# Kernel tuning notes

Hardware: AMD Instinct MI355X
Metric: run time of the kernel (lower is better)

Reference implementation:

```python
import jax, jax.numpy as jnp
import numpy as np

M_RANGE = 3
K = 2 * M_RANGE + 1          # kernel size = 7
N_CLASS = K * K              # 49 motion classes
IM_CHANNEL = 3


def setup_inputs() -> dict:
    key = jax.random.key(0)
    k1, k2, k3, k4 = jax.random.split(key, 4)
    B, H, W = 16, 256, 256
    im_input = jax.random.normal(k1, (B, 2 * IM_CHANNEL, H, W), dtype=jnp.float32)
    im_output = jax.random.normal(k2, (B, IM_CHANNEL, H, W), dtype=jnp.float32)
    # motion in [-M_RANGE, M_RANGE-1) so that floor(m)+M_RANGE+1 <= K-1 (valid bin)
    gt_motion = jax.random.uniform(k3, (B, 2, H, W), dtype=jnp.float32) * (2 * M_RANGE - 1) - M_RANGE
    # grouped-conv weight (already in post-swapaxes [n_class, 1, K, K] layout)
    m_kernel = jax.random.uniform(k4, (N_CLASS, 1, K, K), dtype=jnp.float32)
    return {"im_input": im_input, "im_output": im_output,
            "gt_motion": gt_motion, "m_kernel": m_kernel}


def _axis_weights(m):
    # m: [B,H,W] -> bilinear binning weights over K bins: [B,H,W,K]
    f = jnp.floor(m)
    frac = m - f
    idx = f.astype(jnp.int32) + M_RANGE
    oh0 = jax.nn.one_hot(idx, K, dtype=m.dtype)
    oh1 = jax.nn.one_hot(idx + 1, K, dtype=m.dtype)
    return (1.0 - frac)[..., None] * oh0 + frac[..., None] * oh1


def motion2mask(motion):
    # faithful vectorization of the triple-loop: mask[c=iy*K+ix] = b[iy]*a[ix]
    ax = _axis_weights(motion[:, 0])   # x-motion -> columns of ger(b, a)
    ay = _axis_weights(motion[:, 1])   # y-motion -> rows
    mask = ay[..., :, None] * ax[..., None, :]       # [B,H,W,K,K] outer product
    B, H, W = motion.shape[0], motion.shape[2], motion.shape[3]
    return mask.reshape(B, H, W, N_CLASS).transpose(0, 3, 1, 2)  # [B,N_CLASS,H,W]


def _conv(x, w, groups):
    return jax.lax.conv_general_dilated(
        x, w, window_strides=(1, 1),
        padding=[(M_RANGE, M_RANGE), (M_RANGE, M_RANGE)],
        dimension_numbers=("NCHW", "OIHW", "NCHW"),
        feature_group_count=groups)


def reference(im_input, im_output, gt_motion, m_kernel):
    m_mask = motion2mask(gt_motion)                   # [B,N_CLASS,H,W]
    out_mask = _conv(m_mask, m_kernel, N_CLASS)       # grouped conv, same shape
    im = im_input[:, -IM_CHANNEL:]                    # [B,3,H,W]
    B, C, H, W = im.shape
    # construct_image: each channel expanded to N_CLASS copies then grouped-conv
    # == plain conv of each single channel with all N_CLASS kernels
    nearby = _conv(im.reshape(B * C, 1, H, W), m_kernel, 1)
    nearby = nearby.reshape(B, C, N_CLASS, H, W)
    pred = (nearby * out_mask[:, None]).sum(axis=2)   # [B,3,H,W]
    return pred, m_mask
```

## Files before the change

kernel.cpp:

```cpp
#include <hip/hip_runtime.h>
#include <hip/hip_fp16.h>

typedef _Float16 f16x8 __attribute__((ext_vector_type(8)));
typedef float    f32x4 __attribute__((ext_vector_type(4)));

#define TILE   16
#define HALO   22
#define KK     7
#define NCLASS 49
#define IMW    256
#define IMH    256
#define HW     65536
#define HH     484
#define NV     42
#define WROW   34

#define OFF_OMV    0
#define OFF_HALOF  10752
#define OFF_HALOB  11236
#define OFF_KV     11360
#define SH_TOTAL   13424
#define OFF_IML64  10752
#define OFF_IML32  11720

#define WS_B    0
#define WS_KV   3072
#define WS_KV4  (3072/4)

__device__ __forceinline__ unsigned h2u(__half2 h) { union { __half2 h; unsigned u; } c; c.h = h; return c.u; }
__device__ __forceinline__ __half2  u2h(unsigned u) { union { __half2 h; unsigned u; } c; c.u = u; return c.h; }

__global__ void gtnet_setup(const float* __restrict__ m_kernel, unsigned* __restrict__ ws)
{
    const int tid = threadIdx.x;
    for (int idx = tid; idx < 768; idx += 256) {
        int lane = idx & 63, kitnt = idx >> 6;
        int kit = kitnt >> 2, nt = kitnt & 3;
        int vb0 = (lane >> 4) * 4, tcol = lane & 15;
        int t = nt * 16 + tcol; int tc = (t > 48) ? 48 : t;
        uint4 o;
        unsigned* op = (unsigned*)&o;
        #pragma unroll
        for (int j = 0; j < 4; j++) {
            int v = kit * 16 + vb0 + j;
            float lo = (v <= 41) ? m_kernel[v * NCLASS + tc]        : 0.0f;
            float hi = (v <= 41) ? m_kernel[(v + KK) * NCLASS + tc] : 0.0f;
            op[j] = h2u(__halves2half2(__float2half_rn(lo), __float2half_rn(hi)));
        }
        ((uint4*)ws)[idx] = o;
    }
    for (int i = tid; i < 2064; i += 256) {
        unsigned val = 0u;
        if (i < NCLASS * NV) {
            int s = i / NV, n = i - s * NV;
            val = h2u(__halves2half2(__float2half_rn(m_kernel[n * NCLASS + s]),
                                     __float2half_rn(m_kernel[(n + KK) * NCLASS + s])));
        }
        ws[WS_KV + i] = val;
    }
}

__global__ __launch_bounds__(256, 3)
void gtnet_kernel(const float* __restrict__ im_input,
                  const float* __restrict__ gt_motion,
                  float* __restrict__ out_pred,
                  float* __restrict__ out_mask,
                  const unsigned* __restrict__ ws)
{
    __shared__ __align__(16) unsigned SH[SH_TOTAL];
    unsigned*      const omV    = SH + OFF_OMV;
    unsigned*      const haloF  = SH + OFF_HALOF;
    unsigned char* const haloB8 = (unsigned char*)(SH + OFF_HALOB);
    unsigned*      const KV     = SH + OFF_KV;
    float2*        const iml64  = (float2*)(SH + OFF_IML64);
    float*         const iml32  = (float*)(SH + OFF_IML32);

    const int tid  = threadIdx.x;
    const int lane = tid & 63, wv_id = tid >> 6;
    const int tx = tid & 15, ty = tid >> 4;
    const int x0 = blockIdx.x * TILE, y0 = blockIdx.y * TILE;
    const int b  = blockIdx.z;
    const int x = x0 + tx, y = y0 + ty;

    const float* mot_x = gt_motion + (size_t)b * 2 * HW;
    const float* mot_y = mot_x + HW;
    const float* imP   = im_input + ((size_t)b * 6 + 3) * HW;

    float2 imr01[2]; float imr2[2];
    #pragma unroll
    for (int k = 0; k < 2; k++) {
        int i = tid + k * 256;
        float2 v01 = make_float2(0.0f, 0.0f); float v2 = 0.0f;
        if (i < HH) {
            int hy = i / HALO, hx = i - hy * HALO;
            int gy = y0 - 3 + hy, gx = x0 - 3 + hx;
            if (gy >= 0 && gy < IMH && gx >= 0 && gx < IMW) {
                int off = gy * IMW + gx;
                v01.x = imP[off];
                v01.y = imP[off + HW];
                v2    = imP[off + 2 * HW];
            }
        }
        imr01[k] = v01; imr2[k] = v2;
    }

    {
        const uint4* kvsrc = (const uint4*)(ws + WS_KV);
        uint4*       kvdst = (uint4*)KV;
        for (int i = tid; i < 516; i += 256) kvdst[i] = kvsrc[i];
    }
    #pragma unroll
    for (int k = 0; k < 2; k++) {
        int i = tid + k * 256;
        if (i < HH) {
            int hy = i / HALO, hx = i - hy * HALO;
            int gy = y0 - 3 + hy, gx = x0 - 3 + hx;
            unsigned pf = 0u, n4b = 255u;
            if (gy >= 0 && gy < IMH && gx >= 0 && gx < IMW) {
                int off = gy * IMW + gx;
                float ay = mot_y[off] + 3.0f;
                float ax = mot_x[off] + 3.0f;
                float iyf = floorf(ay), ixf = floorf(ax);
                float fy = ay - iyf,    fx = ax - ixf;
                int n00 = (int)iyf * KK + (int)ixf;
                n00 = (n00 < 0) ? 0 : ((n00 > 40) ? 40 : n00);
                pf  = h2u(__halves2half2(__float2half_rn(fy), __float2half_rn(fx)));
                n4b = (unsigned)(n00 * 4);
            }
            haloF[i]  = pf;
            haloB8[i] = (unsigned char)n4b;
        }
    }
    {
        uint4* p = reinterpret_cast<uint4*>(omV);
        for (int i = tid; i < (2 * NV * 128) / 4; i += 256) p[i] = make_uint4(0, 0, 0, 0);
    }

    __syncthreads();

    {
        int off = y * IMW + x;
        float ay = mot_y[off] + 3.0f;
        float ax = mot_x[off] + 3.0f;
        float iyf = floorf(ay), ixf = floorf(ax);
        float fy = ay - iyf,    fx = ax - ixf;
        int   iy = (int)iyf,    ix = (int)ixf;
        float wyA[KK], wxB[KK];
        #pragma unroll
        for (int a = 0; a < KK; a++) {
            wyA[a] = (a == iy) ? (1.0f - fy) : ((a == iy + 1) ? fy : 0.0f);
            wxB[a] = (a == ix) ? (1.0f - fx) : ((a == ix + 1) ? fx : 0.0f);
        }
        float* mm = out_mask + (size_t)b * NCLASS * HW + off;
        #pragma unroll
        for (int a = 0; a < KK; a++)
            #pragma unroll
            for (int bb = 0; bb < KK; bb++)
                mm[(size_t)(a * KK + bb) * HW] = wyA[a] * wxB[bb];
    }

    unsigned* const omHalf = omV + (tid >> 7) * (NV * 128) + (tid & 127);
    const unsigned c_m11 = 0x3C00BC00u;
    const unsigned c_10  = 0x00003C00u;
    #pragma unroll
    for (int u = 0; u < KK; u++) {
        unsigned pfr[KK], n4r[KK];
        #pragma unroll
        for (int v = 0; v < KK; v++) {
            int q = (ty + u) * HALO + (tx + v);
            pfr[v] = haloF[q];
            n4r[v] = (unsigned)haloB8[q];
        }
        #pragma unroll
        for (int v = 0; v < KK; v++) {
            const int s = u * KK + v;
            unsigned n4u = n4r[v];
            unsigned n4  = (n4u == 255u) ? 0u : n4u;
            unsigned wyb, wx2;
            asm("v_pk_fma_f16 %0, %1, %2, %3 op_sel:[0,0,0] op_sel_hi:[0,1,1]"
                : "=v"(wyb) : "v"(pfr[v]), "v"(c_m11), "v"(c_10));
            asm("v_pk_fma_f16 %0, %1, %2, %3 op_sel:[1,0,0] op_sel_hi:[1,1,1]"
                : "=v"(wx2) : "v"(pfr[v]), "v"(c_m11), "v"(c_10));
            wyb = (n4u == 255u) ? 0u : wyb;
            const unsigned* kp =
                (const unsigned*)((const char*)KV + s * (NV * 4) + n4);
            unsigned kvA = kp[0], kvB = kp[1];
            unsigned* ob = (unsigned*)((char*)omHalf + n4 * 128);
            unsigned o0 = ob[0], o1 = ob[128];
            unsigned tA, tB;
            asm("v_pk_mul_f16 %0, %1, %2 op_sel:[0,0] op_sel_hi:[1,0]"
                : "=v"(tA) : "v"(wyb), "v"(wx2));
            asm("v_pk_mul_f16 %0, %1, %2 op_sel:[0,1] op_sel_hi:[1,1]"
                : "=v"(tB) : "v"(wyb), "v"(wx2));
            __half2 cA = __hmul2(u2h(tA), u2h(kvA));
            __half2 cB = __hmul2(u2h(tB), u2h(kvB));
            ob[0]   = h2u(__hadd2(u2h(o0), cA));
            ob[128] = h2u(__hadd2(u2h(o1), cB));
        }
    }

    __syncthreads();

    uint4 braw[3][4];
    {
        const uint4* bsrc = (const uint4*)(ws + WS_B);
        #pragma unroll
        for (int kit = 0; kit < 3; kit++)
            #pragma unroll
            for (int nt = 0; nt < 4; nt++)
                braw[kit][nt] = bsrc[(kit * 4 + nt) * 64 + lane];
    }

    #pragma unroll
    for (int k = 0; k < 2; k++) {
        int i = tid + k * 256;
        if (i < HH) { iml64[i] = imr01[k]; iml32[i] = imr2[k]; }
    }

    f32x4 acc[4][4];
    #pragma unroll
    for (int mt = 0; mt < 4; mt++)
        #pragma unroll
        for (int nt = 0; nt < 4; nt++)
            acc[mt][nt] = (f32x4){0.0f, 0.0f, 0.0f, 0.0f};

    const int vb0  = (lane >> 4) * 4;
    const int tcol = lane & 15;
    #pragma unroll
    for (int kit = 0; kit < 3; kit++) {
        f16x8 afk[4];
        #pragma unroll
        for (int mt = 0; mt < 4; mt++) {
            int px = wv_id * 64 + mt * 16 + tcol;
            const unsigned* pxb = omV + (px >> 7) * (NV * 128) + (px & 127);
            int vb = kit * 16 + vb0;
            union { unsigned u[4]; f16x8 v; } au;
            #pragma unroll
            for (int j = 0; j < 4; j++) {
                unsigned d = pxb[(vb + j) * 128];
                au.u[j] = (vb + j <= 41) ? d : 0u;
            }
            afk[mt] = au.v;
        }
        #pragma unroll
        for (int mt = 0; mt < 4; mt++) {
            #pragma unroll
            for (int nt = 0; nt < 4; nt++) {
                union { uint4 q; f16x8 v; } bc; bc.q = braw[kit][nt];
                acc[mt][nt] = __builtin_amdgcn_mfma_f32_16x16x32_f16(afk[mt], bc.v, acc[mt][nt], 0, 0, 0);
            }
        }
    }

    __syncthreads();

    #pragma unroll
    for (int mt = 0; mt < 4; mt++) {
        #pragma unroll
        for (int r = 0; r < 4; r++) {
            int px = wv_id * 64 + mt * 16 + (lane >> 4) * 4 + r;
            unsigned* wrow = SH + px * WROW + tcol;
            unsigned v0 = h2u(__halves2half2(__float2half_rn(acc[mt][0][r]),
                                             __float2half_rn(acc[mt][1][r])));
            unsigned v1 = h2u(__halves2half2(__float2half_rn(acc[mt][2][r]),
                                             __float2half_rn(acc[mt][3][r])));
            wrow[0]  = v0;
            wrow[16] = v1;
        }
    }

    __syncthreads();

    union { uint2 q[16]; unsigned d[32]; } wr;
    const uint2* wp = (const uint2*)(SH + tid * WROW);
    #pragma unroll
    for (int c = 0; c < 16; c++) wr.q[c] = wp[c];

    #define WHALF(t) ( (t) < 16 ? __low2half(u2h(wr.d[(t)])) :           \
                       (t) < 32 ? __high2half(u2h(wr.d[(t) - 16])) :     \
                       (t) < 48 ? __low2half(u2h(wr.d[(t) - 16])) :      \
                                  __high2half(u2h(wr.d[16])) )

    float a0 = 0.0f, a1 = 0.0f, a2 = 0.0f;
    #pragma unroll
    for (int p = 0; p < KK; p++) {
        #pragma unroll
        for (int qq = 0; qq < KK; qq++) {
            float wvv = __half2float(WHALF(p * KK + qq));
            int   hq  = (ty + p) * HALO + (tx + qq);
            float2 i01 = iml64[hq];
            float  i2  = iml32[hq];
            a0 = fmaf(wvv, i01.x, a0);
            a1 = fmaf(wvv, i01.y, a1);
            a2 = fmaf(wvv, i2,    a2);
        }
    }
    #undef WHALF
    float* pr = out_pred + (size_t)b * 3 * HW + y * IMW + x;
    pr[0]      = a0;
    pr[HW]     = a1;
    pr[2 * HW] = a2;
}

extern "C" void kernel_launch(void* const* d_in, const int* in_sizes, int n_in,
                              void* d_out, int out_size, void* d_ws, size_t ws_size,
                              hipStream_t stream) {
    const float* im_input  = (const float*)d_in[0];
    const float* gt_motion = (const float*)d_in[2];
    const float* m_kernel  = (const float*)d_in[3];

    float* pred = (float*)d_out;
    float* mask = pred + (size_t)16 * 3 * HW;

    hipLaunchKernelGGL(gtnet_setup, dim3(1), dim3(256), 0, stream,
                       m_kernel, (unsigned*)d_ws);

    dim3 grid(IMW / TILE, IMH / TILE, 16);
    dim3 block(256);
    hipLaunchKernelGGL(gtnet_kernel, grid, block, 0, stream,
                       im_input, gt_motion, pred, mask, (const unsigned*)d_ws);
}
```

Baseline: 329.3 us.

## Read packed kernel-weight pairs from global memory and pack halo data into uint2

Drops the per-block copy of the kernel-weight table into shared memory. Weight pairs are now gathered straight from a global workspace table laid out as uint2 per (class, bin), which the setup kernel precomputes. Motion fractions and bin offsets are packed into one uint2 halo entry, so each tap needs a single LDS read, and the weight gathers are hoisted ahead of the arithmetic. This shrinks shared memory and removes a copy plus LDS traffic, but it trades them for scattered global/L1 gathers inside the hot loop.

```diff
diff --git a/kernel.cpp b/kernel.cpp
--- a/kernel.cpp
+++ b/kernel.cpp
@@ -16,16 +16,13 @@
 #define WROW   34
 
 #define OFF_OMV    0
-#define OFF_HALOF  10752
-#define OFF_HALOB  11236
-#define OFF_KV     11360
-#define SH_TOTAL   13424
+#define OFF_HALO2  10752
+#define SH_TOTAL   12204
 #define OFF_IML64  10752
 #define OFF_IML32  11720
 
 #define WS_B    0
-#define WS_KV   3072
-#define WS_KV4  (3072/4)
+#define WS_KVP  3072
 
 __device__ __forceinline__ unsigned h2u(__half2 h) { union { __half2 h; unsigned u; } c; c.h = h; return c.u; }
 __device__ __forceinline__ __half2  u2h(unsigned u) { union { __half2 h; unsigned u; } c; c.u = u; return c.h; }
@@ -49,14 +46,17 @@
         }
         ((uint4*)ws)[idx] = o;
     }
-    for (int i = tid; i < 2064; i += 256) {
-        unsigned val = 0u;
-        if (i < NCLASS * NV) {
-            int s = i / NV, n = i - s * NV;
-            val = h2u(__halves2half2(__float2half_rn(m_kernel[n * NCLASS + s]),
-                                     __float2half_rn(m_kernel[(n + KK) * NCLASS + s])));
-        }
-        ws[WS_KV + i] = val;
+    uint2* kvp = (uint2*)(ws + WS_KVP);
+    for (int i = tid; i < NCLASS * NV; i += 256) {
+        int s = i / NV, n = i - (i / NV) * NV;
+        float k0 = m_kernel[n * NCLASS + s];
+        float k7 = m_kernel[(n + 7) * NCLASS + s];
+        float k1 = m_kernel[(n + 1) * NCLASS + s];
+        float k8 = (n + 8 <= 48) ? m_kernel[(n + 8) * NCLASS + s] : 0.0f;
+        uint2 o;
+        o.x = h2u(__halves2half2(__float2half_rn(k0), __float2half_rn(k7)));
+        o.y = h2u(__halves2half2(__float2half_rn(k1), __float2half_rn(k8)));
+        kvp[i] = o;
     }
 }
 
@@ -68,12 +68,10 @@
                   const unsigned* __restrict__ ws)
 {
     __shared__ __align__(16) unsigned SH[SH_TOTAL];
-    unsigned*      const omV    = SH + OFF_OMV;
-    unsigned*      const haloF  = SH + OFF_HALOF;
-    unsigned char* const haloB8 = (unsigned char*)(SH + OFF_HALOB);
-    unsigned*      const KV     = SH + OFF_KV;
-    float2*        const iml64  = (float2*)(SH + OFF_IML64);
-    float*         const iml32  = (float*)(SH + OFF_IML32);
+    unsigned* const omV   = SH + OFF_OMV;
+    uint2*    const halo2 = (uint2*)(SH + OFF_HALO2);
+    float2*   const iml64 = (float2*)(SH + OFF_IML64);
+    float*    const iml32 = (float*)(SH + OFF_IML32);
 
     const int tid  = threadIdx.x;
     const int lane = tid & 63, wv_id = tid >> 6;
@@ -104,18 +102,13 @@
         imr01[k] = v01; imr2[k] = v2;
     }
 
-    {
-        const uint4* kvsrc = (const uint4*)(ws + WS_KV);
-        uint4*       kvdst = (uint4*)KV;
-        for (int i = tid; i < 516; i += 256) kvdst[i] = kvsrc[i];
-    }
     #pragma unroll
     for (int k = 0; k < 2; k++) {
         int i = tid + k * 256;
         if (i < HH) {
             int hy = i / HALO, hx = i - hy * HALO;
             int gy = y0 - 3 + hy, gx = x0 - 3 + hx;
-            unsigned pf = 0u, n4b = 255u;
+            unsigned pf = 0u, n8b = 0xFFFFFFFFu;
             if (gy >= 0 && gy < IMH && gx >= 0 && gx < IMW) {
                 int off = gy * IMW + gx;
                 float ay = mot_y[off] + 3.0f;
@@ -125,10 +118,10 @@
                 int n00 = (int)iyf * KK + (int)ixf;
                 n00 = (n00 < 0) ? 0 : ((n00 > 40) ? 40 : n00);
                 pf  = h2u(__halves2half2(__float2half_rn(fy), __float2half_rn(fx)));
-                n4b = (unsigned)(n00 * 4);
+                n8b = (unsigned)(n00 * 8);
             }
-            haloF[i]  = pf;
-            haloB8[i] = (unsigned char)n4b;
+            uint2 hv; hv.x = pf; hv.y = n8b;
+            halo2[i] = hv;
         }
     }
     {
@@ -160,40 +153,41 @@
     }
 
     unsigned* const omHalf = omV + (tid >> 7) * (NV * 128) + (tid & 127);
+    const uint2* const kvpT = (const uint2*)(ws + WS_KVP);
     const unsigned c_m11 = 0x3C00BC00u;
     const unsigned c_10  = 0x00003C00u;
     #pragma unroll
     for (int u = 0; u < KK; u++) {
-        unsigned pfr[KK], n4r[KK];
-        #pragma unroll
-        for (int v = 0; v < KK; v++) {
-            int q = (ty + u) * HALO + (tx + v);
-            pfr[v] = haloF[q];
-            n4r[v] = (unsigned)haloB8[q];
-        }
+        uint2 hvr[KK];
+        #pragma unroll
+        for (int v = 0; v < KK; v++)
+            hvr[v] = halo2[(ty + u) * HALO + (tx + v)];
+        unsigned n8r[KK]; uint2 kvr[KK];
         #pragma unroll
         for (int v = 0; v < KK; v++) {
             const int s = u * KK + v;
-            unsigned n4u = n4r[v];
-            unsigned n4  = (n4u == 255u) ? 0u : n4u;
+            unsigned n8u = hvr[v].y;
+            n8r[v] = (n8u == 0xFFFFFFFFu) ? 0u : n8u;
+            kvr[v] = *(const uint2*)((const char*)(kvpT + s * NV) + n8r[v]);
+        }
+        #pragma unroll
+        for (int v = 0; v < KK; v++) {
+            unsigned pf = hvr[v].x;
             unsigned wyb, wx2;
             asm("v_pk_fma_f16 %0, %1, %2, %3 op_sel:[0,0,0] op_sel_hi:[0,1,1]"
-                : "=v"(wyb) : "v"(pfr[v]), "v"(c_m11), "v"(c_10));
+                : "=v"(wyb) : "v"(pf), "v"(c_m11), "v"(c_10));
             asm("v_pk_fma_f16 %0, %1, %2, %3 op_sel:[1,0,0] op_sel_hi:[1,1,1]"
-                : "=v"(wx2) : "v"(pfr[v]), "v"(c_m11), "v"(c_10));
-            wyb = (n4u == 255u) ? 0u : wyb;
-            const unsigned* kp =
-                (const unsigned*)((const char*)KV + s * (NV * 4) + n4);
-            unsigned kvA = kp[0], kvB = kp[1];
-            unsigned* ob = (unsigned*)((char*)omHalf + n4 * 128);
-            unsigned o0 = ob[0], o1 = ob[128];
+                : "=v"(wx2) : "v"(pf), "v"(c_m11), "v"(c_10));
+            wyb = (hvr[v].y == 0xFFFFFFFFu) ? 0u : wyb;
             unsigned tA, tB;
             asm("v_pk_mul_f16 %0, %1, %2 op_sel:[0,0] op_sel_hi:[1,0]"
                 : "=v"(tA) : "v"(wyb), "v"(wx2));
             asm("v_pk_mul_f16 %0, %1, %2 op_sel:[0,1] op_sel_hi:[1,1]"
                 : "=v"(tB) : "v"(wyb), "v"(wx2));
-            __half2 cA = __hmul2(u2h(tA), u2h(kvA));
-            __half2 cB = __hmul2(u2h(tB), u2h(kvB));
+            unsigned* ob = (unsigned*)((char*)omHalf + n8r[v] * 64);
+            unsigned o0 = ob[0], o1 = ob[128];
+            __half2 cA = __hmul2(u2h(tA), u2h(kvr[v].x));
+            __half2 cB = __hmul2(u2h(tB), u2h(kvr[v].y));
             ob[0]   = h2u(__hadd2(u2h(o0), cA));
             ob[128] = h2u(__hadd2(u2h(o1), cB));
         }
```

Measured after the change: 329.2 us. Within noise of the previous version (-0.0%).
